# Performance work log

Hardware: AMD Instinct MI355X
Metric: run time of the kernel (lower is better)

## Reference

```python
import jax, jax.numpy as jnp
import numpy as np
from jax import lax

B, C_IN, D, H, W = 1, 64, 48, 48, 48
R = 3
PC = 64          # proj_channels
OC = 128         # out_channels
K = (2 * R + 1) ** 3  # 343 offsets
OFFSETS = np.array([(dz, dy, dx)
                    for dz in range(-R, R + 1)
                    for dy in range(-R, R + 1)
                    for dx in range(-R, R + 1)], dtype=np.int32)


def setup_inputs() -> dict:
    key = jax.random.key(0)
    ks = jax.random.split(key, 10)
    s = 0.05
    return {
        'source_features': jax.random.normal(ks[0], (B, C_IN, D, H, W), jnp.float32),
        'warped_target_features': jax.random.normal(ks[1], (B, C_IN, D, H, W), jnp.float32),
        'proj_src_w': jax.random.normal(ks[2], (PC, C_IN, 1, 1, 1), jnp.float32) * s,
        'proj_src_b': jax.random.normal(ks[3], (PC,), jnp.float32) * s,
        'proj_tgt_w': jax.random.normal(ks[4], (PC, C_IN, 1, 1, 1), jnp.float32) * s,
        'proj_tgt_b': jax.random.normal(ks[5], (PC,), jnp.float32) * s,
        'enc1_w': jax.random.normal(ks[6], (OC, K + 3, 3, 3, 3), jnp.float32) * s,
        'enc1_b': jax.random.normal(ks[7], (OC,), jnp.float32) * s,
        'enc2_w': jax.random.normal(ks[8], (OC, OC, 3, 3, 3), jnp.float32) * s,
        'enc2_b': jax.random.normal(ks[9], (OC,), jnp.float32) * s,
    }


def conv3d(x, w, b, pad):
    out = lax.conv_general_dilated(
        x, w, window_strides=(1, 1, 1), padding=[(pad, pad)] * 3,
        dimension_numbers=('NCDHW', 'OIDHW', 'NCDHW'))
    return out + b[None, :, None, None, None]


def l2norm_c(x):
    # torch F.normalize(dim=1): x / max(||x||_2, 1e-12)
    n = jnp.sqrt(jnp.sum(x * x, axis=1, keepdims=True))
    return x / jnp.maximum(n, 1e-12)


def instance_norm(x, eps=1e-5):
    # InstanceNorm3d, affine=False: per (B,C), biased var over D,H,W
    m = jnp.mean(x, axis=(2, 3, 4), keepdims=True)
    v = jnp.var(x, axis=(2, 3, 4), keepdims=True)
    return (x - m) * lax.rsqrt(v + eps)


def reference(source_features, warped_target_features,
              proj_src_w, proj_src_b, proj_tgt_w, proj_tgt_b,
              enc1_w, enc1_b, enc2_w, enc2_b):
    sp = l2norm_c(conv3d(source_features, proj_src_w, proj_src_b, 0))
    tp = l2norm_c(conv3d(warped_target_features, proj_tgt_w, proj_tgt_b, 0))
    padded = jnp.pad(tp, ((0, 0), (0, 0), (R, R), (R, R), (R, R)), mode='edge')
    offs = jnp.asarray(OFFSETS)  # [K,3] int32

    def corr_one(off):
        # shifted window of padded target, dot over channels -> [B,D,H,W]
        shifted = lax.dynamic_slice(
            padded, (0, 0, R + off[0], R + off[1], R + off[2]), sp.shape)
        return jnp.sum(sp * shifted, axis=1)

    corr = lax.map(corr_one, offs)          # [K,B,D,H,W]
    corr = jnp.moveaxis(corr, 0, 1)         # [B,K,D,H,W]

    # online-softmax expected offset == softmax over K weighted by offset vecs
    wts = jax.nn.softmax(corr, axis=1)
    eo = jnp.einsum('bkdhw,kc->bcdhw', wts, offs.astype(sp.dtype))  # [B,3,D,H,W]

    feat = jnp.concatenate([corr, eo], axis=1)  # [B,K+3,D,H,W]
    h = conv3d(feat, enc1_w, enc1_b, 1)
    h = jax.nn.gelu(instance_norm(h), approximate=False)
    h = conv3d(h, enc2_w, enc2_b, 1)
    h = jax.nn.gelu(instance_norm(h), approximate=False)
    return h
```

## Files before the change

### kernel.cpp

```cpp
#include <hip/hip_runtime.h>
#include <math.h>
#include <stdint.h>

#define VOL 110592
#define CINP 64
#define PCH 64

typedef short short8 __attribute__((ext_vector_type(8)));
typedef float floatx4 __attribute__((ext_vector_type(4)));
typedef _Float16 h8 __attribute__((ext_vector_type(8)));
typedef _Float16 h2v __attribute__((ext_vector_type(2)));

__device__ __forceinline__ ushort f2bf(float f) {
    union { float f; uint32_t u; } v; v.f = f;
    uint32_t r = v.u + 0x7FFFu + ((v.u >> 16) & 1u);
    return (ushort)(r >> 16);
}

__device__ __forceinline__ float hdot2(h2v a, h2v b, float c) {
#if __has_builtin(__builtin_amdgcn_fdot2)
    return __builtin_amdgcn_fdot2(a, b, c, false);
#else
    return fmaf((float)a[0], (float)b[0], fmaf((float)a[1], (float)b[1], c));
#endif
}

__global__ __launch_bounds__(256) void proj_l2norm_kernel(
    const float* __restrict__ x,
    const float* __restrict__ w,
    const float* __restrict__ b,
    _Float16* __restrict__ out)
{
    const int v = blockIdx.x * 256 + threadIdx.x;
    float xr[CINP];
    for (int ci = 0; ci < CINP; ci++)
        xr[ci] = x[(size_t)ci * VOL + v];

    float acc[PCH];
    for (int c = 0; c < PCH; c++) {
        float a = b[c];
        #pragma unroll
        for (int ci = 0; ci < CINP; ci++)
            a = fmaf(w[c * CINP + ci], xr[ci], a);
        acc[c] = a;
    }
    float s = 0.f;
    #pragma unroll
    for (int c = 0; c < PCH; c++) s += acc[c] * acc[c];
    const float inv = 1.0f / fmaxf(sqrtf(s), 1e-12f);
    #pragma unroll
    for (int c = 0; c < PCH; c++)
        out[(size_t)v * PCH + c] = (_Float16)(acc[c] * inv);
}

__global__ __launch_bounds__(256) void corr_fused_kernel(
    const _Float16* __restrict__ sp,
    const _Float16* __restrict__ tp,
    ushort* __restrict__ featT)
{
    const int t  = threadIdx.x;
    const int c8 = t & 7;
    const int vg = t >> 3;
    const int v  = blockIdx.x * 32 + vg;
    const int x = v % 48, y = (v / 48) % 48, z = v / 2304;

    __shared__ __align__(16) ushort lds[32 * 360];

    const h8 s = *(const h8*)(sp + (size_t)v * PCH + c8 * 8);

    const bool owner = (c8 < 7);
    const float fdx_own = (float)(c8 - 3);
    float ssum = 0.f, e0 = 0.f, e1 = 0.f;

    int k = 0;
    for (int dz = -3; dz <= 3; dz++) {
        const int zb = min(max(z + dz, 0), 47) * 2304;
        const float fdz = (float)dz;
        for (int dy = -3; dy <= 3; dy++) {
            const int rb = zb + min(max(y + dy, 0), 47) * 48;
            const float fdy = (float)dy;
            h8 tv[7];
            #pragma unroll
            for (int dxi = 0; dxi < 7; dxi++) {
                const int xc = min(max(x + dxi - 3, 0), 47);
                tv[dxi] = *(const h8*)(tp + (size_t)(rb + xc) * PCH + c8 * 8);
            }
            float p[8];
            #pragma unroll
            for (int dxi = 0; dxi < 7; dxi++) {
                const h8 tvv = tv[dxi];
                float d0 = hdot2((h2v){s[0], s[1]}, (h2v){tvv[0], tvv[1]}, 0.f);
                d0 = hdot2((h2v){s[2], s[3]}, (h2v){tvv[2], tvv[3]}, d0);
                float d1 = hdot2((h2v){s[4], s[5]}, (h2v){tvv[4], tvv[5]}, 0.f);
                d1 = hdot2((h2v){s[6], s[7]}, (h2v){tvv[6], tvv[7]}, d1);
                p[dxi] = d0 + d1;
            }
            p[7] = 0.f;

            float r0, r1, r2, r3;
            {
                const bool hi = (c8 & 1);
                float m0 = hi ? p[0] : p[1];
                float m1 = hi ? p[2] : p[3];
                float m2 = hi ? p[4] : p[5];
                float m3 = hi ? p[6] : p[7];
                m0 = __shfl_xor(m0, 1);
                m1 = __shfl_xor(m1, 1);
                m2 = __shfl_xor(m2, 1);
                m3 = __shfl_xor(m3, 1);
                r0 = (hi ? p[1] : p[0]) + m0;
                r1 = (hi ? p[3] : p[2]) + m1;
                r2 = (hi ? p[5] : p[4]) + m2;
                r3 = (hi ? p[7] : p[6]) + m3;
            }
            float q0, q1;
            {
                const bool hi = (c8 & 2);
                float m0 = hi ? r0 : r1;
                float m1 = hi ? r2 : r3;
                m0 = __shfl_xor(m0, 2);
                m1 = __shfl_xor(m1, 2);
                q0 = (hi ? r1 : r0) + m0;
                q1 = (hi ? r3 : r2) + m1;
            }
            float dot;
            {
                const bool hi = (c8 & 4);
                float m0 = hi ? q0 : q1;
                m0 = __shfl_xor(m0, 4);
                dot = (hi ? q1 : q0) + m0;
            }

            if (owner) {
                lds[vg * 360 + k + c8] = f2bf(dot);
                const float e = __expf(dot);
                ssum += e;
                e0 = fmaf(e, fdz, e0);
                e1 = fmaf(e, fdy, e1);
            }
            k += 7;
        }
    }

    float e2 = fdx_own * ssum;
    #pragma unroll
    for (int m = 1; m < 8; m <<= 1) {
        ssum += __shfl_xor(ssum, m);
        e0   += __shfl_xor(e0, m);
        e1   += __shfl_xor(e1, m);
        e2   += __shfl_xor(e2, m);
    }

    if (c8 == 0) {
        const float inv = 1.f / ssum;
        lds[vg * 360 + 343] = f2bf(e0 * inv);
        lds[vg * 360 + 344] = f2bf(e1 * inv);
        lds[vg * 360 + 345] = f2bf(e2 * inv);
        #pragma unroll
        for (int j = 346; j < 352; j++) lds[vg * 360 + j] = 0;
    }
    __syncthreads();

    ushort* ob = featT + (size_t)blockIdx.x * 32 * 352;
    #pragma unroll
    for (int j = 0; j < 6; j++) {
        const int idx = t + j * 256;
        if (idx < 1408) {
            const int row = idx / 44, col = (idx % 44) * 8;
            *(int4*)(ob + (size_t)row * 352 + col) = *(const int4*)(&lds[row * 360 + col]);
        }
    }
}

template<int CIN, int CPAD>
__global__ __launch_bounds__(256) void wprep_kernel(
    const float* __restrict__ w, ushort* __restrict__ wTo, float* __restrict__ zp)
{
    if (blockIdx.x == 0 && threadIdx.x < 4) zp[threadIdx.x] = 0.f;
    const int oc = blockIdx.x;
    for (int idx = threadIdx.x; idx < CPAD * 27; idx += 256) {
        const int icp = idx / 27, tap = idx - icp * 27;
        float val = 0.f;
        if (icp < CIN) val = w[((size_t)oc * CIN + icp) * 27 + tap];
        wTo[((size_t)tap * 128 + oc) * CPAD + icp] = f2bf(val);
    }
}

template<int CPAD>
__global__ __launch_bounds__(256, 2) void conv3_mfma_kernel(
    const ushort* __restrict__ xT,
    const ushort* __restrict__ wT,
    const float* __restrict__ bias,
    const ushort* __restrict__ zpad,
    float* __restrict__ out)
{
    const int blk = (blockIdx.x % 8) * 108 + (blockIdx.x / 8);
    const int tx = blk % 3, ty = (blk / 3) % 12, tz = blk / 36;
    const int x0 = tx * 16, y0 = ty * 4, z0 = tz * 2;
    const int t = threadIdx.x;
    const int wave = t >> 6;
    const int lane = t & 63;
    const int l = lane & 15;
    const int q = lane >> 4;
    const int ocw = (wave & 1) * 64;
    const int mzw = wave >> 1;

    __shared__ __align__(16) ushort win[2][432 * 32];

    int off[7];
    #pragma unroll
    for (int it = 0; it < 7; it++) {
        const int c = wave + it * 4;
        off[it] = -1;
        if (c < 27) {
            const int i = c * 64 + lane;
            const int p = i >> 2, g = i & 3;
            const int wz = p / 108, pr = p - wz * 108;
            const int wy = pr / 18, wx = pr - wy * 18;
            const int gz = z0 + wz - 1, gy = y0 + wy - 1, gx = x0 + wx - 1;
            if ((unsigned)gx < 48u && (unsigned)gy < 48u && (unsigned)gz < 48u)
                off[it] = ((gz * 2304 + gy * 48 + gx) * CPAD + g * 8) * 2;
        }
    }

    floatx4 acc[4][4];
    #pragma unroll
    for (int i = 0; i < 4; i++)
        #pragma unroll
        for (int j = 0; j < 4; j++)
            acc[i][j] = (floatx4){0.f, 0.f, 0.f, 0.f};

    const ushort* wbase = wT + (size_t)(ocw + l) * CPAD + q * 8;
    const int ldsbase = (mzw * 108 + l) * 32 + q * 8;

#define STAGE(CK, BUFP)                                                    \
    {                                                                      \
        const char* xck_ = (const char*)xT + (size_t)(CK) * 64;            \
        _Pragma("unroll")                                                  \
        for (int it_ = 0; it_ < 7; it_++) {                                \
            const int c_ = wave + it_ * 4;                                 \
            if (c_ < 27) {                                                 \
                const ushort* gp_ = (off[it_] >= 0)                        \
                    ? (const ushort*)(xck_ + off[it_]) : zpad;             \
                __builtin_amdgcn_global_load_lds(                          \
                    (const __attribute__((address_space(1))) uint32_t*)gp_,\
                    (__attribute__((address_space(3))) uint32_t*)((BUFP) + c_ * 512 + lane * 8), \
                    16, 0, 0);                                             \
            }                                                              \
        }                                                                  \
    }

    const int NCH = CPAD / 32;

    STAGE(0, &win[0][0]);
    __syncthreads();

    #pragma unroll 1
    for (int ck = 0; ck < NCH; ck++) {
        const ushort* cbuf = &win[ck & 1][0];
        ushort* nbuf = &win[(ck + 1) & 1][0];
        const ushort* wck = wbase + ck * 32;

        short8 A0[4], A1[4];
        A0[0] = *(const short8*)(wck);
        A0[1] = *(const short8*)(wck + 16 * CPAD);
        A0[2] = *(const short8*)(wck + 32 * CPAD);
        A0[3] = *(const short8*)(wck + 48 * CPAD);

        short8 B0[4], B1[4];
        B0[0] = *(const short8*)(&cbuf[ldsbase +    0]);
        B0[1] = *(const short8*)(&cbuf[ldsbase +  576]);
        B0[2] = *(const short8*)(&cbuf[ldsbase + 1152]);
        B0[3] = *(const short8*)(&cbuf[ldsbase + 1728]);

        if (ck + 1 < NCH) STAGE(ck + 1, nbuf);

#define CONV_BODY(TP, AU, AL, BU, BL)                                      \
        {                                                                  \
            const int tpn_ = (TP) + 1;                                     \
            if (tpn_ < 27) {                                               \
                const ushort* wp_ = wck + (size_t)tpn_ * (128 * CPAD);     \
                AL[0] = *(const short8*)(wp_);                             \
                AL[1] = *(const short8*)(wp_ + 16 * CPAD);                 \
                AL[2] = *(const short8*)(wp_ + 32 * CPAD);                 \
                AL[3] = *(const short8*)(wp_ + 48 * CPAD);                 \
                const int dzn_ = tpn_ / 9;                                 \
                const int dyn_ = (tpn_ / 3) % 3;                           \
                const int dxn_ = tpn_ % 3;                                 \
                const int pbn_ = ldsbase + (dzn_ * 108 + dyn_ * 18 + dxn_) * 32; \
                BL[0] = *(const short8*)(&cbuf[pbn_ +    0]);              \
                BL[1] = *(const short8*)(&cbuf[pbn_ +  576]);              \
                BL[2] = *(const short8*)(&cbuf[pbn_ + 1152]);              \
                BL[3] = *(const short8*)(&cbuf[pbn_ + 1728]);              \
            }                                                              \
            acc[0][0] = __builtin_amdgcn_mfma_f32_16x16x32_bf16(AU[0], BU[0], acc[0][0], 0, 0, 0); \
            acc[1][0] = __builtin_amdgcn_mfma_f32_16x16x32_bf16(AU[1], BU[0], acc[1][0], 0, 0, 0); \
            acc[2][0] = __builtin_amdgcn_mfma_f32_16x16x32_bf16(AU[2], BU[0], acc[2][0], 0, 0, 0); \
            acc[3][0] = __builtin_amdgcn_mfma_f32_16x16x32_bf16(AU[3], BU[0], acc[3][0], 0, 0, 0); \
            acc[0][1] = __builtin_amdgcn_mfma_f32_16x16x32_bf16(AU[0], BU[1], acc[0][1], 0, 0, 0); \
            acc[1][1] = __builtin_amdgcn_mfma_f32_16x16x32_bf16(AU[1], BU[1], acc[1][1], 0, 0, 0); \
            acc[2][1] = __builtin_amdgcn_mfma_f32_16x16x32_bf16(AU[2], BU[1], acc[2][1], 0, 0, 0); \
            acc[3][1] = __builtin_amdgcn_mfma_f32_16x16x32_bf16(AU[3], BU[1], acc[3][1], 0, 0, 0); \
            acc[0][2] = __builtin_amdgcn_mfma_f32_16x16x32_bf16(AU[0], BU[2], acc[0][2], 0, 0, 0); \
            acc[1][2] = __builtin_amdgcn_mfma_f32_16x16x32_bf16(AU[1], BU[2], acc[1][2], 0, 0, 0); \
            acc[2][2] = __builtin_amdgcn_mfma_f32_16x16x32_bf16(AU[2], BU[2], acc[2][2], 0, 0, 0); \
            acc[3][2] = __builtin_amdgcn_mfma_f32_16x16x32_bf16(AU[3], BU[2], acc[3][2], 0, 0, 0); \
            acc[0][3] = __builtin_amdgcn_mfma_f32_16x16x32_bf16(AU[0], BU[3], acc[0][3], 0, 0, 0); \
            acc[1][3] = __builtin_amdgcn_mfma_f32_16x16x32_bf16(AU[1], BU[3], acc[1][3], 0, 0, 0); \
            acc[2][3] = __builtin_amdgcn_mfma_f32_16x16x32_bf16(AU[2], BU[3], acc[2][3], 0, 0, 0); \
            acc[3][3] = __builtin_amdgcn_mfma_f32_16x16x32_bf16(AU[3], BU[3], acc[3][3], 0, 0, 0); \
        }

        #pragma unroll 1
        for (int tg = 0; tg < 13; tg++) {
            const int tp = tg * 2;
            CONV_BODY(tp, A0, A1, B0, B1);
            CONV_BODY(tp + 1, A1, A0, B1, B0);
        }
        CONV_BODY(26, A0, A1, B0, B1);
#undef CONV_BODY

        __syncthreads();
    }
#undef STAGE

    #pragma unroll
    for (int nt = 0; nt < 4; nt++) {
        const int ocb = ocw + nt * 16 + q * 4;
        const float4 bv = *(const float4*)(bias + ocb);
        #pragma unroll
        for (int mt = 0; mt < 4; mt++) {
            const int v = (z0 + mzw) * 2304 + (y0 + mt) * 48 + x0 + l;
            out[(size_t)(ocb + 0) * VOL + v] = acc[nt][mt][0] + bv.x;
            out[(size_t)(ocb + 1) * VOL + v] = acc[nt][mt][1] + bv.y;
            out[(size_t)(ocb + 2) * VOL + v] = acc[nt][mt][2] + bv.z;
            out[(size_t)(ocb + 3) * VOL + v] = acc[nt][mt][3] + bv.w;
        }
    }
}

__global__ __launch_bounds__(256) void chan_stats_part_kernel(
    const float* __restrict__ x, float* __restrict__ pstats )
{
    const int c = blockIdx.x, g = blockIdx.y;
    const float4* p = (const float4*)(x + (size_t)c * VOL) + g * 3456;
    float s = 0.f, s2 = 0.f;
    #pragma unroll
    for (int j = 0; j < 14; j++) {
        const int i = threadIdx.x + j * 256;
        if (i < 3456) {
            const float4 v = p[i];
            s += v.x + v.y + v.z + v.w;
            s2 = fmaf(v.x, v.x, fmaf(v.y, v.y, fmaf(v.z, v.z, fmaf(v.w, v.w, s2))));
        }
    }
    s  += __shfl_down(s, 32);  s  += __shfl_down(s, 16);
    s  += __shfl_down(s, 8);   s  += __shfl_down(s, 4);
    s  += __shfl_down(s, 2);   s  += __shfl_down(s, 1);
    s2 += __shfl_down(s2, 32); s2 += __shfl_down(s2, 16);
    s2 += __shfl_down(s2, 8);  s2 += __shfl_down(s2, 4);
    s2 += __shfl_down(s2, 2);  s2 += __shfl_down(s2, 1);
    __shared__ float rs[4], rs2[4];
    if ((threadIdx.x & 63) == 0) {
        rs[threadIdx.x >> 6] = s;
        rs2[threadIdx.x >> 6] = s2;
    }
    __syncthreads();
    if (threadIdx.x == 0) {
        pstats[(c * 8 + g) * 2]     = rs[0] + rs[1] + rs[2] + rs[3];
        pstats[(c * 8 + g) * 2 + 1] = rs2[0] + rs2[1] + rs2[2] + rs2[3];
    }
}

__global__ __launch_bounds__(128) void chan_stats_fin_kernel(
    const float* __restrict__ pstats, float* __restrict__ stats )
{
    const int c = threadIdx.x;
    float s = 0.f, s2 = 0.f;
    #pragma unroll
    for (int g = 0; g < 8; g++) {
        s  += pstats[(c * 8 + g) * 2];
        s2 += pstats[(c * 8 + g) * 2 + 1];
    }
    const float mean = s / (float)VOL;
    const float var  = s2 / (float)VOL - mean * mean;
    stats[c * 2]     = mean;
    stats[c * 2 + 1] = rsqrtf(var + 1e-5f);
}

__device__ __forceinline__ float gelu_exact(float h)
{
    return 0.5f * h * (1.f + erff(h * 0.70710678118654752f));
}

__global__ __launch_bounds__(256) void norm_gelu_kernel(
    const float* __restrict__ x, const float* __restrict__ stats,
    float* __restrict__ out)
{
    const size_t i = (size_t)blockIdx.x * 256 + threadIdx.x;
    const int c = (int)(i / (VOL / 4));
    const float mean = stats[c * 2], rstd = stats[c * 2 + 1];
    const float4 xv = ((const float4*)x)[i];
    float4 o;
    o.x = gelu_exact((xv.x - mean) * rstd);
    o.y = gelu_exact((xv.y - mean) * rstd);
    o.z = gelu_exact((xv.z - mean) * rstd);
    o.w = gelu_exact((xv.w - mean) * rstd);
    ((float4*)out)[i] = o;
}

__global__ __launch_bounds__(256) void norm_gelu_transpose_kernel(
    const float* __restrict__ x, const float* __restrict__ stats,
    ushort* __restrict__ outT)
{
    __shared__ float tile[32][33];
    const int v0 = blockIdx.x * 32;
    const int c0 = blockIdx.y * 32;
    const int t = threadIdx.x;
    const int vl = t & 31, cl = t >> 5;
    #pragma unroll
    for (int i = 0; i < 4; i++) {
        const int c = c0 + cl + i * 8;
        const float mean = stats[c * 2], rstd = stats[c * 2 + 1];
        const float val = x[(size_t)c * VOL + v0 + vl];
        tile[cl + i * 8][vl] = gelu_exact((val - mean) * rstd);
    }
    __syncthreads();
    const int vw = t >> 3, cg = t & 7;
    ushort4 o;
    o.x = f2bf(tile[cg * 4 + 0][vw]);
    o.y = f2bf(tile[cg * 4 + 1][vw]);
    o.z = f2bf(tile[cg * 4 + 2][vw]);
    o.w = f2bf(tile[cg * 4 + 3][vw]);
    *(ushort4*)(outT + (size_t)(v0 + vw) * 128 + c0 + cg * 4) = o;
}

extern "C" void kernel_launch(void* const* d_in, const int* in_sizes, int n_in,
                              void* d_out, int out_size, void* d_ws, size_t ws_size,
                              hipStream_t stream)
{
    const float* src = (const float*)d_in[0];
    const float* tgt = (const float*)d_in[1];
    const float* psw = (const float*)d_in[2];
    const float* psb = (const float*)d_in[3];
    const float* ptw = (const float*)d_in[4];
    const float* ptb = (const float*)d_in[5];
    const float* e1w = (const float*)d_in[6];
    const float* e1b = (const float*)d_in[7];
    const float* e2w = (const float*)d_in[8];
    const float* e2b = (const float*)d_in[9];

    float* ws = (float*)d_ws;
    _Float16* sp  = (_Float16*)ws;
    _Float16* tp  = (_Float16*)(ws + (size_t)32 * VOL);
    ushort* featT = (ushort*)(ws + (size_t)128 * VOL);
    float*  h1    = ws;
    float*  h2    = ws + (size_t)128 * VOL;
    ushort* h1T   = (ushort*)(ws + (size_t)304 * VOL);
    float*  w1Tf  = ws + (size_t)368 * VOL;
    ushort* w1T   = (ushort*)w1Tf;
    float*  w2Tf  = w1Tf + 608256;
    ushort* w2T   = (ushort*)w2Tf;
    float*  stats = w2Tf + 221184;
    float*  pstats = stats + 256;
    float*  zpadf  = pstats + 2048;
    const ushort* zpad = (const ushort*)zpadf;

    wprep_kernel<346, 352><<<128, 256, 0, stream>>>(e1w, w1T, zpadf);
    wprep_kernel<128, 128><<<128, 256, 0, stream>>>(e2w, w2T, zpadf);

    proj_l2norm_kernel<<<432, 256, 0, stream>>>(src, psw, psb, sp);
    proj_l2norm_kernel<<<432, 256, 0, stream>>>(tgt, ptw, ptb, tp);
    corr_fused_kernel<<<3456, 256, 0, stream>>>(sp, tp, featT);

    conv3_mfma_kernel<352><<<864, 256, 0, stream>>>(featT, w1T, e1b, zpad, h1);
    chan_stats_part_kernel<<<dim3(128, 8), 256, 0, stream>>>(h1, pstats);
    chan_stats_fin_kernel<<<1, 128, 0, stream>>>(pstats, stats);
    norm_gelu_transpose_kernel<<<dim3(3456, 4), 256, 0, stream>>>(h1, stats, h1T);

    conv3_mfma_kernel<128><<<864, 256, 0, stream>>>(h1T, w2T, e2b, zpad, h2);
    chan_stats_part_kernel<<<dim3(128, 8), 256, 0, stream>>>(h2, pstats);
    chan_stats_fin_kernel<<<1, 128, 0, stream>>>(pstats, stats);
    norm_gelu_kernel<<<(128 * VOL) / 1024, 256, 0, stream>>>(h2, stats, (float*)d_out);
}
```

Before: 1.019 ms.

## Compute correlation volume with MFMA tiles over 16-voxel x-rows

Replaces the per-voxel fdot2 correlation kernel with a one-wavefront kernel that treats 16 consecutive x-voxels as an MFMA A tile. For each (dz,dy) row it multiplies that tile against 32 neighbouring target voxels, then picks the valid 7 dx diagonals per voxel. This removes the cross-lane shuffle reductions and the repeated per-voxel target loads. In exchange most MFMA outputs are discarded (7 of 32 per row), and the smaller 64-thread blocks may change occupancy.

```diff
diff --git a/kernel.cpp b/kernel.cpp
--- a/kernel.cpp
+++ b/kernel.cpp
@@ -9,20 +9,11 @@
 typedef short short8 __attribute__((ext_vector_type(8)));
 typedef float floatx4 __attribute__((ext_vector_type(4)));
 typedef _Float16 h8 __attribute__((ext_vector_type(8)));
-typedef _Float16 h2v __attribute__((ext_vector_type(2)));
 
 __device__ __forceinline__ ushort f2bf(float f) {
     union { float f; uint32_t u; } v; v.f = f;
     uint32_t r = v.u + 0x7FFFu + ((v.u >> 16) & 1u);
     return (ushort)(r >> 16);
-}
-
-__device__ __forceinline__ float hdot2(h2v a, h2v b, float c) {
-#if __has_builtin(__builtin_amdgcn_fdot2)
-    return __builtin_amdgcn_fdot2(a, b, c, false);
-#else
-    return fmaf((float)a[0], (float)b[0], fmaf((float)a[1], (float)b[1], c));
-#endif
 }
 
 __global__ __launch_bounds__(256) void proj_l2norm_kernel(
@@ -53,122 +44,132 @@
         out[(size_t)v * PCH + c] = (_Float16)(acc[c] * inv);
 }
 
-__global__ __launch_bounds__(256) void corr_fused_kernel(
+__global__ __launch_bounds__(64) void corr_mfma_kernel(
     const _Float16* __restrict__ sp,
     const _Float16* __restrict__ tp,
     ushort* __restrict__ featT)
 {
-    const int t  = threadIdx.x;
-    const int c8 = t & 7;
-    const int vg = t >> 3;
-    const int v  = blockIdx.x * 32 + vg;
-    const int x = v % 48, y = (v / 48) % 48, z = v / 2304;
-
-    __shared__ __align__(16) ushort lds[32 * 360];
-
-    const h8 s = *(const h8*)(sp + (size_t)v * PCH + c8 * 8);
-
-    const bool owner = (c8 < 7);
-    const float fdx_own = (float)(c8 - 3);
-    float ssum = 0.f, e0 = 0.f, e1 = 0.f;
-
-    int k = 0;
-    for (int dz = -3; dz <= 3; dz++) {
-        const int zb = min(max(z + dz, 0), 47) * 2304;
-        const float fdz = (float)dz;
-        for (int dy = -3; dy <= 3; dy++) {
-            const int rb = zb + min(max(y + dy, 0), 47) * 48;
-            const float fdy = (float)dy;
-            h8 tv[7];
+    const int v0 = blockIdx.x * 16;
+    const int x0 = v0 % 48;
+    const int y  = (v0 / 48) % 48;
+    const int z  = v0 / 2304;
+    const int lane = threadIdx.x;
+    const int l = lane & 15;
+    const int q = lane >> 4;
+
+    __shared__ __align__(16) ushort lds[16 * 352];
+
+    const _Float16* ap = sp + (size_t)(v0 + l) * 64 + q * 8;
+    const h8 Afrag0 = *(const h8*)(ap);
+    const h8 Afrag1 = *(const h8*)(ap + 32);
+
+    const int xc0 = min(max(x0 - 8 + l, 0), 47);
+    const int xc1 = min(max(x0 + 8 + l, 0), 47);
+
+    int  ldsoff[4];
+    float fdx[4];
+    int  vva[4], vsel[4];
+    #pragma unroll
+    for (int r = 0; r < 4; r++) {
+        const int x = q * 4 + r;
+        const int dx0 = l - 8 - x;
+        const int dx1 = l + 8 - x;
+        const int va = ((unsigned)(dx0 + 3) <= 6u);
+        const int vb = ((unsigned)(dx1 + 3) <= 6u);
+        const int dxs = va ? dx0 : dx1;
+        vsel[r] = va;
+        vva[r] = va | vb;
+        fdx[r] = (float)dxs;
+        ldsoff[r] = x * 352 + (dxs + 3);
+    }
+
+    float ssum[4] = {0.f, 0.f, 0.f, 0.f};
+    float e0a[4]  = {0.f, 0.f, 0.f, 0.f};
+    float e1a[4]  = {0.f, 0.f, 0.f, 0.f};
+    float e2a[4]  = {0.f, 0.f, 0.f, 0.f};
+
+#define LOADB(BV, RR)                                                      \
+    {                                                                      \
+        const int rr_ = (RR);                                              \
+        const int zc_ = min(max(z + rr_ / 7 - 3, 0), 47);                  \
+        const int yc_ = min(max(y + rr_ % 7 - 3, 0), 47);                  \
+        const size_t rb_ = (size_t)(zc_ * 2304 + yc_ * 48);                \
+        const _Float16* p0_ = tp + (rb_ + xc0) * 64 + q * 8;               \
+        const _Float16* p1_ = tp + (rb_ + xc1) * 64 + q * 8;               \
+        BV[0] = *(const h8*)(p0_);                                         \
+        BV[1] = *(const h8*)(p0_ + 32);                                    \
+        BV[2] = *(const h8*)(p1_);                                         \
+        BV[3] = *(const h8*)(p1_ + 32);                                    \
+    }
+
+#define ROW_BODY(RR, BU)                                                   \
+    {                                                                      \
+        const floatx4 z4_ = {0.f, 0.f, 0.f, 0.f};                          \
+        floatx4 aA_ = __builtin_amdgcn_mfma_f32_16x16x32_f16(Afrag0, BU[0], z4_, 0, 0, 0); \
+        aA_ = __builtin_amdgcn_mfma_f32_16x16x32_f16(Afrag1, BU[1], aA_, 0, 0, 0); \
+        floatx4 aB_ = __builtin_amdgcn_mfma_f32_16x16x32_f16(Afrag0, BU[2], z4_, 0, 0, 0); \
+        aB_ = __builtin_amdgcn_mfma_f32_16x16x32_f16(Afrag1, BU[3], aB_, 0, 0, 0); \
+        const int rr_ = (RR);                                              \
+        const float fdz_ = (float)(rr_ / 7 - 3);                           \
+        const float fdy_ = (float)(rr_ % 7 - 3);                           \
+        const int kb_ = rr_ * 7;                                           \
+        _Pragma("unroll")                                                  \
+        for (int r = 0; r < 4; r++) {                                      \
+            const float val_ = vsel[r] ? aA_[r] : aB_[r];                  \
+            const float e_ = vva[r] ? __expf(val_) : 0.f;                  \
+            ssum[r] += e_;                                                 \
+            e0a[r] = fmaf(e_, fdz_, e0a[r]);                               \
+            e1a[r] = fmaf(e_, fdy_, e1a[r]);                               \
+            e2a[r] = fmaf(e_, fdx[r], e2a[r]);                             \
+            if (vva[r]) lds[ldsoff[r] + kb_] = f2bf(val_);                 \
+        }                                                                  \
+    }
+
+    h8 B0[4], B1[4];
+    LOADB(B0, 0)
+    #pragma unroll 1
+    for (int g = 0; g < 24; g++) {
+        const int r0 = g * 2;
+        LOADB(B1, r0 + 1)
+        ROW_BODY(r0, B0)
+        LOADB(B0, r0 + 2)
+        ROW_BODY(r0 + 1, B1)
+    }
+    ROW_BODY(48, B0)
+#undef ROW_BODY
+#undef LOADB
+
+    #pragma unroll
+    for (int m = 1; m <= 8; m <<= 1) {
+        #pragma unroll
+        for (int r = 0; r < 4; r++) {
+            ssum[r] += __shfl_xor(ssum[r], m);
+            e0a[r]  += __shfl_xor(e0a[r], m);
+            e1a[r]  += __shfl_xor(e1a[r], m);
+            e2a[r]  += __shfl_xor(e2a[r], m);
+        }
+    }
+
+    if (l == 0) {
+        #pragma unroll
+        for (int r = 0; r < 4; r++) {
+            const float inv = 1.f / ssum[r];
+            const int b = (q * 4 + r) * 352;
+            lds[b + 343] = f2bf(e0a[r] * inv);
+            lds[b + 344] = f2bf(e1a[r] * inv);
+            lds[b + 345] = f2bf(e2a[r] * inv);
             #pragma unroll
-            for (int dxi = 0; dxi < 7; dxi++) {
-                const int xc = min(max(x + dxi - 3, 0), 47);
-                tv[dxi] = *(const h8*)(tp + (size_t)(rb + xc) * PCH + c8 * 8);
-            }
-            float p[8];
-            #pragma unroll
-            for (int dxi = 0; dxi < 7; dxi++) {
-                const h8 tvv = tv[dxi];
-                float d0 = hdot2((h2v){s[0], s[1]}, (h2v){tvv[0], tvv[1]}, 0.f);
-                d0 = hdot2((h2v){s[2], s[3]}, (h2v){tvv[2], tvv[3]}, d0);
-                float d1 = hdot2((h2v){s[4], s[5]}, (h2v){tvv[4], tvv[5]}, 0.f);
-                d1 = hdot2((h2v){s[6], s[7]}, (h2v){tvv[6], tvv[7]}, d1);
-                p[dxi] = d0 + d1;
-            }
-            p[7] = 0.f;
-
-            float r0, r1, r2, r3;
-            {
-                const bool hi = (c8 & 1);
-                float m0 = hi ? p[0] : p[1];
-                float m1 = hi ? p[2] : p[3];
-                float m2 = hi ? p[4] : p[5];
-                float m3 = hi ? p[6] : p[7];
-                m0 = __shfl_xor(m0, 1);
-                m1 = __shfl_xor(m1, 1);
-                m2 = __shfl_xor(m2, 1);
-                m3 = __shfl_xor(m3, 1);
-                r0 = (hi ? p[1] : p[0]) + m0;
-                r1 = (hi ? p[3] : p[2]) + m1;
-                r2 = (hi ? p[5] : p[4]) + m2;
-                r3 = (hi ? p[7] : p[6]) + m3;
-            }
-            float q0, q1;
-            {
-                const bool hi = (c8 & 2);
-                float m0 = hi ? r0 : r1;
-                float m1 = hi ? r2 : r3;
-                m0 = __shfl_xor(m0, 2);
-                m1 = __shfl_xor(m1, 2);
-                q0 = (hi ? r1 : r0) + m0;
-                q1 = (hi ? r3 : r2) + m1;
-            }
-            float dot;
-            {
-                const bool hi = (c8 & 4);
-                float m0 = hi ? q0 : q1;
-                m0 = __shfl_xor(m0, 4);
-                dot = (hi ? q1 : q0) + m0;
-            }
-
-            if (owner) {
-                lds[vg * 360 + k + c8] = f2bf(dot);
-                const float e = __expf(dot);
-                ssum += e;
-                e0 = fmaf(e, fdz, e0);
-                e1 = fmaf(e, fdy, e1);
-            }
-            k += 7;
-        }
-    }
-
-    float e2 = fdx_own * ssum;
-    #pragma unroll
-    for (int m = 1; m < 8; m <<= 1) {
-        ssum += __shfl_xor(ssum, m);
-        e0   += __shfl_xor(e0, m);
-        e1   += __shfl_xor(e1, m);
-        e2   += __shfl_xor(e2, m);
-    }
-
-    if (c8 == 0) {
-        const float inv = 1.f / ssum;
-        lds[vg * 360 + 343] = f2bf(e0 * inv);
-        lds[vg * 360 + 344] = f2bf(e1 * inv);
-        lds[vg * 360 + 345] = f2bf(e2 * inv);
-        #pragma unroll
-        for (int j = 346; j < 352; j++) lds[vg * 360 + j] = 0;
+            for (int j = 346; j < 352; j++) lds[b + j] = 0;
+        }
     }
     __syncthreads();
 
-    ushort* ob = featT + (size_t)blockIdx.x * 32 * 352;
-    #pragma unroll
-    for (int j = 0; j < 6; j++) {
-        const int idx = t + j * 256;
-        if (idx < 1408) {
-            const int row = idx / 44, col = (idx % 44) * 8;
-            *(int4*)(ob + (size_t)row * 352 + col) = *(const int4*)(&lds[row * 360 + col]);
-        }
+    ushort* ob = featT + (size_t)v0 * 352;
+    #pragma unroll
+    for (int j = 0; j < 11; j++) {
+        const int idx = lane + j * 64;
+        const int row = idx / 44, col = (idx % 44) * 8;
+        *(int4*)(ob + (size_t)row * 352 + col) = *(const int4*)(&lds[row * 352 + col]);
     }
 }
 
@@ -471,7 +472,7 @@
 
     proj_l2norm_kernel<<<432, 256, 0, stream>>>(src, psw, psb, sp);
     proj_l2norm_kernel<<<432, 256, 0, stream>>>(tgt, ptw, ptb, tp);
-    corr_fused_kernel<<<3456, 256, 0, stream>>>(sp, tp, featT);
+    corr_mfma_kernel<<<VOL / 16, 64, 0, stream>>>(sp, tp, featT);
 
     conv3_mfma_kernel<352><<<864, 256, 0, stream>>>(featT, w1T, e1b, zpad, h1);
     chan_stats_part_kernel<<<dim3(128, 8), 256, 0, stream>>>(h1, pstats);
```

New measurement: 1.027 ms. Within noise of the previous version (+0.7%).
